# Optimization experiments

Measured on AMD Instinct MI355X. Metric: run time of the kernel, lower is better.

## Reference

```python
import jax, jax.numpy as jnp
import numpy as np

N_NODES = 20000
N_EDGES = 320000
IN_F = 16
OUT_F = 16
EDGE_DIM = 16
EDGE_HID = 64
BN_EPS = 1e-5


def setup_inputs() -> dict:
    key = jax.random.key(0)
    ks = jax.random.split(key, 12)
    inp = {
        "h_neigh": jax.random.normal(ks[0], (N_NODES, IN_F), dtype=jnp.float32),
        "h_self": jax.random.normal(ks[1], (N_NODES, IN_F), dtype=jnp.float32),
        "edge_features": jax.random.normal(ks[2], (N_EDGES, EDGE_DIM), dtype=jnp.float32),
        "src": jax.random.randint(ks[3], (N_EDGES,), 0, N_NODES),
        "dst": jax.random.randint(ks[4], (N_EDGES,), 0, N_NODES),
        # params (xavier-ish scale)
        "W_self": jax.random.normal(ks[5], (IN_F, OUT_F), dtype=jnp.float32) * (2.0 / (IN_F + OUT_F)) ** 0.5,
        "bn_gamma": jnp.ones((OUT_F,), dtype=jnp.float32),
        "bn_beta": jnp.zeros((OUT_F,), dtype=jnp.float32),
        "We1": jax.random.normal(ks[6], (EDGE_DIM, EDGE_HID), dtype=jnp.float32) * (2.0 / (EDGE_DIM + EDGE_HID)) ** 0.5,
        "be1": jnp.zeros((EDGE_HID,), dtype=jnp.float32),
        "We2": jax.random.normal(ks[7], (EDGE_HID, IN_F * OUT_F), dtype=jnp.float32) * (2.0 / (EDGE_HID + IN_F * OUT_F)) ** 0.5,
        "be2": jnp.zeros((IN_F * OUT_F,), dtype=jnp.float32),
    }
    return inp


def reference(h_neigh, h_self, edge_features, src, dst,
              W_self, bn_gamma, bn_beta, We1, be1, We2, be2):
    n_nodes = h_self.shape[0]
    in_f, out_f = W_self.shape
    # edge MLP -> per-edge weight matrix [E, in_f, out_f]
    eh = jax.nn.relu(edge_features @ We1 + be1)
    edge_w = (eh @ We2 + be2).reshape(-1, in_f, out_f)
    # gather src features, per-edge matvec, scatter-sum to dst
    # (sum over in_f commutes with the edge sum-reduce, matching
    #  update_all(u_mul_e, sum) followed by .sum(dim=1))
    msg = jnp.einsum('ei,eio->eo', h_neigh[src], edge_w)  # [E, out_f]
    neigh = jax.ops.segment_sum(msg, dst, num_segments=n_nodes)  # [N, out_f]
    # fc_self: Linear(no bias) -> BatchNorm1d (training stats) -> tanh
    y = h_self @ W_self
    mu = y.mean(axis=0)
    var = y.var(axis=0)
    y = (y - mu) / jnp.sqrt(var + BN_EPS) * bn_gamma + bn_beta
    y = jnp.tanh(y)
    z = jax.nn.relu(y + neigh)
    z_norm = jnp.linalg.norm(z, axis=1, keepdims=True)
    z_norm = jnp.where(z_norm == 0, jnp.ones_like(z_norm), z_norm)
    return z / z_norm
```

## Files before the change

### kernel.cpp

```cpp
#include <hip/hip_runtime.h>
#include <hip/hip_bf16.h>
#include <math.h>

#define NN 20000
#define NE 320000
#define BN_EPS 1e-5f
#define CAP 48
#define CNTP 16

#define MSG_BYTES   (NN * CAP * 16 * 4)
#define SLOT_OFF    MSG_BYTES
#define SLOT_BYTES  (NE * 4)
#define CNT_OFF     (SLOT_OFF + SLOT_BYTES)
#define CNT_BYTES   (NN * CNTP * 4)
#define BNACC_OFF   (CNT_OFF + CNT_BYTES)
#define EXTRA_OFF   (BNACC_OFF + 128)
#define EXTRA_BYTES (NN * 16 * 4)
#define Y_OFF       (EXTRA_OFF + EXTRA_BYTES)
#define ZERO_OFF    CNT_OFF
#define ZERO_BYTES  (CNT_BYTES + 128 + EXTRA_BYTES)

typedef _Float16 f16x8 __attribute__((ext_vector_type(8)));
typedef float    f32x4 __attribute__((ext_vector_type(4)));

union H8 { f16x8 v; unsigned short us[8]; unsigned int ui[4]; };

__device__ __forceinline__ unsigned short f2h(float f) {
    _Float16 h = (_Float16)f;
    return __builtin_bit_cast(unsigned short, h);
}
__device__ __forceinline__ unsigned int pack2h(float a, float b) {
    return (unsigned int)f2h(a) | ((unsigned int)f2h(b) << 16);
}

__global__ __launch_bounds__(256) void bucket_kernel(
    const int* __restrict__ dst, int* __restrict__ slot, int* __restrict__ cntp)
{
    int i = (int)blockIdx.x * 256 + (int)threadIdx.x;
    if (i < NE) {
        int d0 = dst[i];
        int k0 = atomicAdd(&cntp[d0 * CNTP], 1);
        slot[i] = k0;
    }
}

__global__ __launch_bounds__(256, 3) void edge_kernel(
    const float* __restrict__ h_neigh, const float* __restrict__ efeat,
    const int* __restrict__ src, const int* __restrict__ dst,
    const int* __restrict__ slot,
    const float* __restrict__ We1, const float* __restrict__ be1,
    const float* __restrict__ We2, const float* __restrict__ be2,
    float* __restrict__ msgb, float* __restrict__ extra,
    const float* __restrict__ h_self, const float* __restrict__ Wsf,
    float* __restrict__ y, float* __restrict__ bnacc)
{
    __shared__ __align__(16) unsigned short A3sw[16 * 2 * 64 * 8];
    __shared__ float red[4][32];

    const int t = threadIdx.x;

    {
#pragma unroll
        for (int i = 0; i < 8; i++) {
            int R = t + 256 * i;
            int co = R & 15;
            int g  = (R >> 4) & 3;
            int mbkb = R >> 6;
            int mb = mbkb >> 1, kb = mbkb & 1;
            const float* wp = We2 + (size_t)(kb * 32 + g * 8) * 256 + mb * 16 + co;
            H8 h8;
#pragma unroll
            for (int j = 0; j < 8; j++)
                h8.us[j] = f2h(wp[j * 256]);
            *(f16x8*)&A3sw[R * 8] = h8.v;
        }
    }
    __syncthreads();

    const int L = t & 63, wv = t >> 6;
    const int lo16 = L & 15, q = L >> 4;
    const int qc = q & 1;
    const bool qlow = (q < 2);
    const bool qhi1 = ((q >> 1) != 0);

    H8 w1[4];
#pragma unroll
    for (int c = 0; c < 4; c++) {
#pragma unroll
        for (int j = 0; j < 8; j++) {
            float w;
            if (q < 2)                 w = We1[(q * 8 + j) * 64 + c * 16 + lo16];
            else if (q == 2 && j == 0) w = be1[c * 16 + lo16];
            else                       w = 0.f;
            w1[c].us[j] = f2h(w);
        }
    }

    H8 be2T;
#pragma unroll
    for (int j = 0; j < 8; j++) {
        float bv = be2[(qc * 8 + j) * 16 + lo16];
        be2T.us[j] = qlow ? f2h(bv) : (unsigned short)0;
    }

    const int addrA = (((q & 1) * 2 + 0) * 16 + lo16) * 4;
    const int addrB = (((q & 1) * 2 + 1) * 16 + lo16) * 4;

    const int NT = NE / 64;
    int bt = blockIdx.x;
    {
        int e = bt * 64 + wv * 16 + lo16;
        int se = src[e];
        int de = dst[e];
        int sl = slot[e];
        const float4* ep0 = (const float4*)(efeat + (size_t)e * 16 + qc * 8);
        float4 efA = ep0[0], efB = ep0[1];
        float xr[16];
        {
            const float4* xp = (const float4*)(h_neigh + (size_t)se * 16);
#pragma unroll
            for (int k4 = 0; k4 < 4; k4++) {
                float4 a = xp[k4];
                xr[k4*4+0] = a.x; xr[k4*4+1] = a.y; xr[k4*4+2] = a.z; xr[k4*4+3] = a.w;
            }
        }

        while (true) {
            int btn = bt + gridDim.x;
            bool hn = btn < NT;
            int en = 0, sen = 0, den = 0, sln = 0;
            float4 efAn = efA, efBn = efB;
            if (hn) {
                en = btn * 64 + wv * 16 + lo16;
                sen = src[en];
                den = dst[en];
                sln = slot[en];
                const float4* epn = (const float4*)(efeat + (size_t)en * 16 + qc * 8);
                efAn = epn[0]; efBn = epn[1];
            }

            H8 a2;
            {
                float ev[8] = {efA.x, efA.y, efA.z, efA.w, efB.x, efB.y, efB.z, efB.w};
#pragma unroll
                for (int j = 0; j < 8; j++) {
                    if (qlow) {
                        a2.us[j] = f2h(ev[j]);
                    } else {
                        a2.us[j] = (q == 2 && j == 0) ? (unsigned short)0x3C00 : (unsigned short)0;
                    }
                }
            }

            float vch[4][4];
#pragma unroll
            for (int c = 0; c < 4; c++) {
                f32x4 c2 = {0.f, 0.f, 0.f, 0.f};
                c2 = __builtin_amdgcn_mfma_f32_16x16x32_f16(w1[c].v, a2.v, c2, 0, 0, 0);
#pragma unroll
                for (int r = 0; r < 4; r++) vch[c][r] = fmaxf(c2[r], 0.f);
            }

            unsigned int dw[4][2];
#pragma unroll
            for (int c = 0; c < 4; c++) {
#pragma unroll
                for (int d = 0; d < 2; d++)
                    dw[c][d] = pack2h(vch[c][2*d], vch[c][2*d+1]);
            }

            H8 b3[2];
#pragma unroll
            for (int kb = 0; kb < 2; kb++) {
#pragma unroll
                for (int tt = 0; tt < 4; tt++) {
                    int d = tt & 1;
                    int addr = (tt >> 1) ? addrB : addrA;
                    int h0 = __builtin_amdgcn_ds_bpermute(addr, (int)dw[kb*2+0][d]);
                    int h1 = __builtin_amdgcn_ds_bpermute(addr, (int)dw[kb*2+1][d]);
                    b3[kb].ui[tt] = (unsigned int)(qhi1 ? h1 : h0);
                }
            }

            float4 nx0 = make_float4(0.f, 0.f, 0.f, 0.f), nx1 = nx0, nx2 = nx0, nx3 = nx0;
            if (hn) {
                const float4* xpn = (const float4*)(h_neigh + (size_t)sen * 16);
                nx0 = xpn[0]; nx1 = xpn[1]; nx2 = xpn[2]; nx3 = xpn[3];
            }

            H8 xT;
#pragma unroll
            for (int j = 0; j < 8; j++)
                xT.us[j] = qlow ? f2h(xr[qc * 8 + j]) : (unsigned short)0;
            f32x4 msg = {0.f, 0.f, 0.f, 0.f};
            msg = __builtin_amdgcn_mfma_f32_16x16x32_f16(be2T.v, xT.v, msg, 0, 0, 0);

#pragma unroll 4
            for (int mb = 0; mb < 16; mb++) {
                f16x8 a3a = *(const f16x8*)&A3sw[((mb * 2 + 0) * 64 + L) * 8];
                f16x8 a3b = *(const f16x8*)&A3sw[((mb * 2 + 1) * 64 + L) * 8];
                f32x4 acc = {0.f, 0.f, 0.f, 0.f};
                acc = __builtin_amdgcn_mfma_f32_16x16x32_f16(a3a, b3[0].v, acc, 0, 0, 0);
                acc = __builtin_amdgcn_mfma_f32_16x16x32_f16(a3b, b3[1].v, acc, 0, 0, 0);
                float xm = xr[mb];
                msg[0] += xm * acc[0];
                msg[1] += xm * acc[1];
                msg[2] += xm * acc[2];
                msg[3] += xm * acc[3];
            }

            if (sl < CAP) {
                *(float4*)(msgb + ((size_t)de * CAP + sl) * 16 + q * 4) =
                    make_float4(msg[0], msg[1], msg[2], msg[3]);
            } else {
                float* xp2 = extra + (size_t)de * 16 + q * 4;
#pragma unroll
                for (int r = 0; r < 4; r++) atomicAdd(xp2 + r, msg[r]);
            }

            if (!hn) break;
            bt = btn; e = en; se = sen; de = den; sl = sln; efA = efAn; efB = efBn;
            xr[0]  = nx0.x; xr[1]  = nx0.y; xr[2]  = nx0.z; xr[3]  = nx0.w;
            xr[4]  = nx1.x; xr[5]  = nx1.y; xr[6]  = nx1.z; xr[7]  = nx1.w;
            xr[8]  = nx2.x; xr[9]  = nx2.y; xr[10] = nx2.z; xr[11] = nx2.w;
            xr[12] = nx3.x; xr[13] = nx3.y; xr[14] = nx3.z; xr[15] = nx3.w;
        }
    }

    int sb = (int)blockIdx.x - 945;
    if (sb >= 0 && sb < 79) {
        int n = sb * 256 + t;
        bool act = (n < NN);
        float hv[16], yv[16];
        if (act) {
            const float4* h4 = (const float4*)(h_self + (size_t)n * 16);
#pragma unroll
            for (int k = 0; k < 4; k++) {
                float4 a = h4[k];
                hv[4*k+0] = a.x; hv[4*k+1] = a.y; hv[4*k+2] = a.z; hv[4*k+3] = a.w;
            }
        } else {
#pragma unroll
            for (int i = 0; i < 16; i++) hv[i] = 0.f;
        }
#pragma unroll
        for (int o = 0; o < 16; o++) {
            float a = 0.f;
#pragma unroll
            for (int i = 0; i < 16; i++) a += hv[i] * Wsf[i*16 + o];
            yv[o] = a;
        }
        if (act) {
            float4* y4 = (float4*)(y + (size_t)n * 16);
#pragma unroll
            for (int k = 0; k < 4; k++)
                y4[k] = make_float4(yv[4*k+0], yv[4*k+1], yv[4*k+2], yv[4*k+3]);
        }
        int lane = t & 63;
#pragma unroll
        for (int o = 0; o < 16; o++) {
            float a = act ? yv[o] : 0.f;
            float b = act ? yv[o]*yv[o] : 0.f;
#pragma unroll
            for (int off = 32; off > 0; off >>= 1) {
                a += __shfl_down(a, off);
                b += __shfl_down(b, off);
            }
            if (lane == 0) { red[wv][o] = a; red[wv][16 + o] = b; }
        }
        __syncthreads();
        if (t < 32) {
            float s = red[0][t] + red[1][t] + red[2][t] + red[3][t];
            atomicAdd(&bnacc[t], s);
        }
    }
}

__global__ __launch_bounds__(256) void final_kernel(
    const float* __restrict__ msgb, const int* __restrict__ cntp,
    const float* __restrict__ extra,
    const float* __restrict__ y, const float* __restrict__ bnacc,
    const float* __restrict__ gamma, const float* __restrict__ beta,
    float* __restrict__ out)
{
    int tb = blockIdx.x * 256 + threadIdx.x;
    int n = tb >> 4;
    if (n >= NN) return;
    int sub = tb & 15, s = sub >> 2, c = sub & 3;

    int deg = cntp[n * CNTP];
    int m = deg < CAP ? deg : CAP;
    const float4* base = (const float4*)(msgb + (size_t)n * CAP * 16);

    float ax = 0.f, ay = 0.f, az = 0.f, aw = 0.f;
    for (int k = s; k < m; k += 4) {
        float4 a0 = base[k * 4 + c];
        ax += a0.x; ay += a0.y; az += a0.z; aw += a0.w;
    }

    ax += __shfl_xor(ax, 4); ax += __shfl_xor(ax, 8);
    ay += __shfl_xor(ay, 4); ay += __shfl_xor(ay, 8);
    az += __shfl_xor(az, 4); az += __shfl_xor(az, 8);
    aw += __shfl_xor(aw, 4); aw += __shfl_xor(aw, 8);

    if (s != 0) return;

    if (deg > CAP) {
        const float4 a0 = *(const float4*)(extra + (size_t)n * 16 + c * 4);
        ax += a0.x; ay += a0.y; az += a0.z; aw += a0.w;
    }

    float4 yv4 = ((const float4*)y)[(size_t)n * 4 + c];
    float yv[4] = {yv4.x, yv4.y, yv4.z, yv4.w};
    float nb[4] = {ax, ay, az, aw};

    const float inv_n = 1.f / (float)NN;
    float z[4];
    float ss = 0.f;
#pragma unroll
    for (int r = 0; r < 4; r++) {
        int o = c * 4 + r;
        float mu  = bnacc[o] * inv_n;
        float var = bnacc[16 + o] * inv_n - mu * mu;
        float inv = rsqrtf(var + BN_EPS);
        float yy  = (yv[r] - mu) * inv * gamma[o] + beta[o];
        float tt  = tanhf(yy);
        float zz  = fmaxf(tt + nb[r], 0.f);
        z[r] = zz;
        ss += zz * zz;
    }
    ss += __shfl_xor(ss, 1);
    ss += __shfl_xor(ss, 2);
    float nrm = sqrtf(ss);
    if (nrm == 0.f) nrm = 1.f;
    float rr = 1.f / nrm;
    *(float4*)(out + (size_t)n * 16 + c * 4) =
        make_float4(z[0]*rr, z[1]*rr, z[2]*rr, z[3]*rr);
}

extern "C" void kernel_launch(void* const* d_in, const int* in_sizes, int n_in,
                              void* d_out, int out_size, void* d_ws, size_t ws_size,
                              hipStream_t stream) {
    const float* h_neigh = (const float*)d_in[0];
    const float* h_self  = (const float*)d_in[1];
    const float* efeat   = (const float*)d_in[2];
    const int*   src     = (const int*)d_in[3];
    const int*   dst     = (const int*)d_in[4];
    const float* W_self  = (const float*)d_in[5];
    const float* gamma   = (const float*)d_in[6];
    const float* beta    = (const float*)d_in[7];
    const float* We1     = (const float*)d_in[8];
    const float* be1     = (const float*)d_in[9];
    const float* We2     = (const float*)d_in[10];
    const float* be2     = (const float*)d_in[11];
    float* out = (float*)d_out;

    char* ws = (char*)d_ws;
    float* msgb  = (float*)ws;
    int*   slot  = (int*)(ws + SLOT_OFF);
    int*   cntp  = (int*)(ws + CNT_OFF);
    float* bnacc = (float*)(ws + BNACC_OFF);
    float* extra = (float*)(ws + EXTRA_OFF);
    float* y     = (float*)(ws + Y_OFF);

    hipMemsetAsync(ws + ZERO_OFF, 0, ZERO_BYTES, stream);

    bucket_kernel<<<(NE + 255) / 256, 256, 0, stream>>>(dst, slot, cntp);
    edge_kernel<<<1024, 256, 0, stream>>>(
        h_neigh, efeat, src, dst, slot, We1, be1, We2, be2,
        msgb, extra, h_self, W_self, y, bnacc);
    final_kernel<<<(NN * 16 + 255) / 256, 256, 0, stream>>>(
        msgb, cntp, extra, y, bnacc, gamma, beta, out);
}
```

Baseline: 146.8 us.

## Fuse destination bucketing atomics into the edge kernel prologue

Removes the separate bucket kernel and its global slot array. Each edge block now does the per-destination atomicAdd for all of its tiles up front and keeps the slots in shared memory indexed by iteration. This saves one kernel launch and a round trip of the slot array through global memory. The atomics now sit in the edge kernel prologue before the main loop, and the shared buffer assumes at most 5 tiles per block (NT=5000 with 1024 blocks).

```diff
diff --git a/kernel.cpp b/kernel.cpp
--- a/kernel.cpp
+++ b/kernel.cpp
@@ -9,9 +9,7 @@
 #define CNTP 16
 
 #define MSG_BYTES   (NN * CAP * 16 * 4)
-#define SLOT_OFF    MSG_BYTES
-#define SLOT_BYTES  (NE * 4)
-#define CNT_OFF     (SLOT_OFF + SLOT_BYTES)
+#define CNT_OFF     MSG_BYTES
 #define CNT_BYTES   (NN * CNTP * 4)
 #define BNACC_OFF   (CNT_OFF + CNT_BYTES)
 #define EXTRA_OFF   (BNACC_OFF + 128)
@@ -33,31 +31,24 @@
     return (unsigned int)f2h(a) | ((unsigned int)f2h(b) << 16);
 }
 
-__global__ __launch_bounds__(256) void bucket_kernel(
-    const int* __restrict__ dst, int* __restrict__ slot, int* __restrict__ cntp)
-{
-    int i = (int)blockIdx.x * 256 + (int)threadIdx.x;
-    if (i < NE) {
-        int d0 = dst[i];
-        int k0 = atomicAdd(&cntp[d0 * CNTP], 1);
-        slot[i] = k0;
-    }
-}
-
 __global__ __launch_bounds__(256, 3) void edge_kernel(
     const float* __restrict__ h_neigh, const float* __restrict__ efeat,
     const int* __restrict__ src, const int* __restrict__ dst,
-    const int* __restrict__ slot,
     const float* __restrict__ We1, const float* __restrict__ be1,
     const float* __restrict__ We2, const float* __restrict__ be2,
     float* __restrict__ msgb, float* __restrict__ extra,
+    int* __restrict__ cntp,
     const float* __restrict__ h_self, const float* __restrict__ Wsf,
     float* __restrict__ y, float* __restrict__ bnacc)
 {
     __shared__ __align__(16) unsigned short A3sw[16 * 2 * 64 * 8];
     __shared__ float red[4][32];
+    __shared__ int elsd[5][64];
 
     const int t = threadIdx.x;
+    const int L = t & 63, wv = t >> 6;
+    const int lo16 = L & 15, q = L >> 4;
+    const int jidx = wv * 16 + lo16;
 
     {
 #pragma unroll
@@ -75,10 +66,21 @@
             *(f16x8*)&A3sw[R * 8] = h8.v;
         }
     }
+
+    const int NT = NE / 64;
+    {
+        int it = 0;
+        for (int btt = (int)blockIdx.x; btt < NT; btt += (int)gridDim.x, ++it) {
+            int e0 = btt * 64 + jidx;
+            if (q == 0) {
+                int d0 = dst[e0];
+                int k0 = atomicAdd(&cntp[d0 * CNTP], 1);
+                elsd[it][jidx] = k0;
+            }
+        }
+    }
     __syncthreads();
 
-    const int L = t & 63, wv = t >> 6;
-    const int lo16 = L & 15, q = L >> 4;
     const int qc = q & 1;
     const bool qlow = (q < 2);
     const bool qhi1 = ((q >> 1) != 0);
@@ -106,13 +108,13 @@
     const int addrA = (((q & 1) * 2 + 0) * 16 + lo16) * 4;
     const int addrB = (((q & 1) * 2 + 1) * 16 + lo16) * 4;
 
-    const int NT = NE / 64;
     int bt = blockIdx.x;
     {
-        int e = bt * 64 + wv * 16 + lo16;
+        int it = 0;
+        int e = bt * 64 + jidx;
         int se = src[e];
         int de = dst[e];
-        int sl = slot[e];
+        int sl = elsd[0][jidx];
         const float4* ep0 = (const float4*)(efeat + (size_t)e * 16 + qc * 8);
         float4 efA = ep0[0], efB = ep0[1];
         float xr[16];
@@ -131,10 +133,10 @@
             int en = 0, sen = 0, den = 0, sln = 0;
             float4 efAn = efA, efBn = efB;
             if (hn) {
-                en = btn * 64 + wv * 16 + lo16;
+                en = btn * 64 + jidx;
                 sen = src[en];
                 den = dst[en];
-                sln = slot[en];
+                sln = elsd[it + 1][jidx];
                 const float4* epn = (const float4*)(efeat + (size_t)en * 16 + qc * 8);
                 efAn = epn[0]; efBn = epn[1];
             }
@@ -220,6 +222,7 @@
 
             if (!hn) break;
             bt = btn; e = en; se = sen; de = den; sl = sln; efA = efAn; efB = efBn;
+            ++it;
             xr[0]  = nx0.x; xr[1]  = nx0.y; xr[2]  = nx0.z; xr[3]  = nx0.w;
             xr[4]  = nx1.x; xr[5]  = nx1.y; xr[6]  = nx1.z; xr[7]  = nx1.w;
             xr[8]  = nx2.x; xr[9]  = nx2.y; xr[10] = nx2.z; xr[11] = nx2.w;
@@ -357,7 +360,6 @@
 
     char* ws = (char*)d_ws;
     float* msgb  = (float*)ws;
-    int*   slot  = (int*)(ws + SLOT_OFF);
     int*   cntp  = (int*)(ws + CNT_OFF);
     float* bnacc = (float*)(ws + BNACC_OFF);
     float* extra = (float*)(ws + EXTRA_OFF);
@@ -365,10 +367,9 @@
 
     hipMemsetAsync(ws + ZERO_OFF, 0, ZERO_BYTES, stream);
 
-    bucket_kernel<<<(NE + 255) / 256, 256, 0, stream>>>(dst, slot, cntp);
     edge_kernel<<<1024, 256, 0, stream>>>(
-        h_neigh, efeat, src, dst, slot, We1, be1, We2, be2,
-        msgb, extra, h_self, W_self, y, bnacc);
+        h_neigh, efeat, src, dst, We1, be1, We2, be2,
+        msgb, extra, cntp, h_self, W_self, y, bnacc);
     final_kernel<<<(NN * 16 + 255) / 256, 256, 0, stream>>>(
         msgb, cntp, extra, y, bnacc, gamma, beta, out);
 }
```

Result: faster. 142.9 us (-2.7%).
